# Optimization experiments

Hardware: AMD Instinct MI355X
Metric: run time of the kernel (lower is better)

## Reference

```python
import jax, jax.numpy as jnp
import numpy as np

EMB = 32
STEPS = 3
SLOPE = 0.01  # LeakyReLU default negative slope


def lrelu(x):
    return jnp.where(x > 0, x, SLOPE * x)


def seg_softmax(logits, seg, num_seg):
    # numerically stable per-segment softmax (matches torch_geometric.utils.softmax)
    m = jax.ops.segment_max(logits, seg, num_segments=num_seg)
    e = jnp.exp(logits - m[seg])
    s = jax.ops.segment_sum(e, seg, num_segments=num_seg)
    return e / s[seg]


def setup_inputs() -> dict:
    key = jax.random.key(0)
    ks = jax.random.split(key, 32)
    N, E, G = 200000, 3200000, 128
    p = lambda k, shape: (jax.random.normal(k, shape, dtype=jnp.float32) * 0.1)
    inp = {
        "node_feats": jax.random.normal(ks[0], (N, 1), dtype=jnp.float32),
        "edge_index": jax.random.randint(ks[1], (2, E), 0, N),
        "batch": jnp.sort(jax.random.randint(ks[2], (N,), 0, G)),
        "num_graphs": G,
        # embed_node: Linear(1, 32)
        "W_embed": p(ks[3], (1, EMB)), "b_embed": p(ks[4], (EMB,)),
        # per-step GraphNet params (stacked over steps)
        "Wm": p(ks[5], (STEPS, EMB, EMB)), "bm": p(ks[6], (STEPS, EMB)),          # f_mess (edge_size=0)
        "Wa": p(ks[7], (STEPS, 3 * EMB, EMB)), "ba": p(ks[8], (STEPS, EMB)),      # f_agg: [x, xg, agg]
        # per-step GlobalNode params
        "Wgate": p(ks[9], (STEPS, EMB, 1)), "bgate": p(ks[10], (STEPS, 1)),       # att_mask
        "Wfeat": p(ks[11], (STEPS, EMB, EMB)), "bfeat": p(ks[12], (STEPS, EMB)),  # att_feat
        "Wt": p(ks[13], (STEPS, 2 * EMB, EMB)), "bt": p(ks[14], (STEPS, EMB)),    # transform
        # heads
        "W_v": p(ks[15], (EMB, 1)), "b_v": p(ks[16], (1,)),
        "W_a0": p(ks[17], (EMB, 2)), "b_a0": p(ks[18], (2,)),
        "W_a1": p(ks[19], (EMB, 1)), "b_a1": p(ks[20], (1,)),
    }
    return inp


def reference(node_feats, edge_index, batch, num_graphs,
              W_embed, b_embed, Wm, bm, Wa, ba, Wgate, bgate, Wfeat, bfeat,
              Wt, bt, W_v, b_v, W_a0, b_a0, W_a1, b_a1):
    N = node_feats.shape[0]
    src, dst = edge_index[0], edge_index[1]

    x = lrelu(node_feats @ W_embed + b_embed)            # [N, 32]
    xg = jnp.zeros((num_graphs, EMB), dtype=x.dtype)     # [G, 32]

    for i in range(Wm.shape[0]):
        # GraphNet: gather -> MLP -> scatter-max -> update MLP + residual
        msg = lrelu(x[src] @ Wm[i] + bm[i])              # [E, 32]
        agg = jax.ops.segment_max(msg, dst, num_segments=N)
        agg = jnp.where(jnp.isfinite(agg), agg, 0.0)     # empty segments -> 0
        z = jnp.concatenate([x, xg[batch], agg], axis=1)  # [N, 96]
        x = lrelu(z @ Wa[i] + ba[i]) + x

        # GlobalNode: GlobalAttention pooling + transform with residual
        gate = seg_softmax((x @ Wgate[i] + bgate[i])[:, 0], batch, num_graphs)  # [N]
        feat = lrelu(x @ Wfeat[i] + bfeat[i])            # [N, 32]
        pooled = jax.ops.segment_sum(gate[:, None] * feat, batch, num_segments=num_graphs)
        cat = jnp.concatenate([pooled, xg], axis=1)      # [G, 64]
        xg = lrelu(cat @ Wt[i] + bt[i]) + xg

    value = xg @ W_v + b_v                               # [G, 1]
    a0_probs = jax.nn.softmax(xg @ W_a0 + b_a0, axis=1)  # [G, 2]
    a1_softmax = seg_softmax((x @ W_a1 + b_a1)[:, 0], batch, num_graphs)  # [N]
    return value, a0_probs, a1_softmax
```

## Files before the change

kernel.cpp:

```cpp
#include <hip/hip_runtime.h>
#include <hip/hip_bf16.h>

#define GG 128
#define SLOPE 0.01f
#define CHUNK 8192
#define NPB 64
#define NREP 64

#define OFF_Wm   0
#define OFF_bm   3072
#define OFF_Wa   3168
#define OFF_ba   12384
#define OFF_Wg   12480
#define OFF_bg   12576
#define OFF_Wf   12592
#define OFF_bf   15664
#define OFF_Wt   15760
#define OFF_bt   21904
#define OFF_Wa1  22000
#define OFF_ba1  22032
#define WCAT_N   22048

__device__ __forceinline__ float lrelu(float v) { return v > 0.f ? v : SLOPE * v; }

__device__ __forceinline__ float ldf(const void* p, int i, int isf) {
    if (isf) return ((const float*)p)[i];
    return __bfloat162float(((const __hip_bfloat16*)p)[i]);
}
__device__ __forceinline__ void stf(void* p, int i, float v, int isf) {
    if (isf) ((float*)p)[i] = v;
    else ((__hip_bfloat16*)p)[i] = __float2bfloat16(v);
}

__device__ __forceinline__ float bfLo(unsigned u) { return __uint_as_float(u << 16); }
__device__ __forceinline__ float bfHi(unsigned u) { return __uint_as_float(u & 0xFFFF0000u); }

__global__ void k_detect(const unsigned short* __restrict__ w, int n, int* __restrict__ flag) {
    __shared__ int bad;
    if (threadIdx.x == 0) bad = 0;
    __syncthreads();
    for (int t = threadIdx.x; t < n; t += 256) {
        unsigned short u = w[t];
        int e = (u >> 7) & 0xFF;
        if (e >= 141) bad = 1;
    }
    __syncthreads();
    if (threadIdx.x == 0) { flag[0] = bad; flag[32] = 1; }
}

struct CvtArgs {
    const void* p[12];
    int off[12];
    int n[12];
};
__global__ void k_cvt_all(CvtArgs a, float* __restrict__ dst, const int* __restrict__ dtf) {
    int isf = *dtf;
    int seg = blockIdx.y;
    int i = blockIdx.x * 256 + threadIdx.x;
    if (i < a.n[seg]) dst[a.off[seg] + i] = ldf(a.p[seg], i, isf);
}

__global__ void k_xgw0(const void* __restrict__ ba0, float* __restrict__ xgw,
                       const int* __restrict__ dtf) {
    int isf = *dtf;
    int idx = blockIdx.x * 256 + threadIdx.x;
    xgw[idx] = ldf(ba0, idx & 31, isf);
}

__global__ void k_embed_msg(const void* __restrict__ nf, const void* __restrict__ We,
                            const void* __restrict__ be,
                            const float* __restrict__ Wm0, const float* __restrict__ bm0,
                            float* __restrict__ x, __hip_bfloat16* __restrict__ m, int N,
                            const int* __restrict__ dtf) {
    __shared__ float WL[1024];
    __shared__ float WeL[32], beL[32], bmL[32];
    __shared__ float xs[8][32];
    int isf = *dtf;
    int tid = threadIdx.x;
    for (int t = tid; t < 1024; t += 256) WL[t] = Wm0[t];
    if (tid < 32) { WeL[tid] = ldf(We, tid, isf); beL[tid] = ldf(be, tid, isf); bmL[tid] = bm0[tid]; }
    int s = tid >> 5, j = tid & 31;
    int n = blockIdx.x * 8 + s;
    __syncthreads();
    float xv = 0.f;
    if (n < N) {
        xv = lrelu(ldf(nf, n, isf) * WeL[j] + beL[j]);
        x[n * 32 + j] = xv;
        xs[s][j] = xv;
    }
    __syncthreads();
    if (n >= N) return;
    float acc = bmL[j];
#pragma unroll
    for (int k = 0; k < 32; ++k) acc += xs[s][k] * WL[k * 32 + j];
    m[n * 32 + j] = __float2bfloat16(lrelu(acc));
}

__global__ void k_graph_off(const int* __restrict__ batch, int* __restrict__ goff, int N) {
    int n = blockIdx.x * 256 + threadIdx.x;
    if (n >= N) return;
    int bn = batch[n];
    if (n == 0) {
        for (int g = 0; g <= bn; ++g) goff[g] = 0;
    } else {
        int bp = batch[n - 1];
        for (int g = bp + 1; g <= bn; ++g) goff[g] = n;
    }
    if (n == N - 1) {
        for (int g = bn + 1; g <= GG; ++g) goff[g] = N;
    }
}

__global__ void k_hist(const int* __restrict__ dst, unsigned* __restrict__ deg, int E) {
    int e = blockIdx.x * 256 + threadIdx.x;
    if (e >= E) return;
    atomicAdd(&deg[dst[e]], 1u);
}
__global__ void k_scan1(const unsigned* __restrict__ deg, unsigned* __restrict__ excl,
                        unsigned* __restrict__ bsum, int N) {
    __shared__ unsigned s[256];
    int i = blockIdx.x * 256 + threadIdx.x;
    unsigned v = (i < N) ? deg[i] : 0u;
    s[threadIdx.x] = v;
    __syncthreads();
    for (int off = 1; off < 256; off <<= 1) {
        unsigned t = (threadIdx.x >= (unsigned)off) ? s[threadIdx.x - off] : 0u;
        __syncthreads();
        s[threadIdx.x] += t;
        __syncthreads();
    }
    if (i < N) excl[i] = s[threadIdx.x] - v;
    if (threadIdx.x == 255) bsum[blockIdx.x] = s[255];
}
__global__ void k_scan2(const unsigned* __restrict__ bsum, unsigned* __restrict__ boff, int nb) {
    __shared__ unsigned s[256];
    __shared__ unsigned carry;
    if (threadIdx.x == 0) carry = 0u;
    __syncthreads();
    for (int base = 0; base < nb; base += 256) {
        int i = base + threadIdx.x;
        unsigned v = (i < nb) ? bsum[i] : 0u;
        s[threadIdx.x] = v;
        __syncthreads();
        for (int off = 1; off < 256; off <<= 1) {
            unsigned t = (threadIdx.x >= (unsigned)off) ? s[threadIdx.x - off] : 0u;
            __syncthreads();
            s[threadIdx.x] += t;
            __syncthreads();
        }
        if (i < nb) boff[i] = carry + s[threadIdx.x] - v;
        __syncthreads();
        if (threadIdx.x == 0) carry += s[255];
        __syncthreads();
    }
}
__global__ void k_scan3(unsigned* __restrict__ indptr, const unsigned* __restrict__ boff,
                        unsigned* __restrict__ cursor, int N, int E) {
    int i = blockIdx.x * 256 + threadIdx.x;
    if (i >= N) return;
    unsigned v = indptr[i] + boff[i >> 8];
    indptr[i] = v;
    cursor[i] = v;
    if (i == 0) indptr[N] = (unsigned)E;
}
__global__ void k_scatter(const int* __restrict__ src, const int* __restrict__ dst,
                          unsigned* __restrict__ cursor, unsigned* __restrict__ ssrc, int E) {
    int e = blockIdx.x * 256 + threadIdx.x;
    if (e >= E) return;
    unsigned pos = atomicAdd(&cursor[dst[e]], 1u);
    ssrc[pos] = (unsigned)src[e];
}

__global__ void k_bhist(const int* __restrict__ dst, unsigned* __restrict__ bcnt, int E, int B) {
    __shared__ unsigned h[2048];
    for (int t = threadIdx.x; t < B; t += 256) h[t] = 0;
    __syncthreads();
    int start = blockIdx.x * CHUNK, end = min(E, start + CHUNK);
    for (int e = start + threadIdx.x; e < end; e += 256)
        atomicAdd(&h[dst[e] >> 8], 1u);
    __syncthreads();
    for (int t = threadIdx.x; t < B; t += 256)
        if (h[t]) atomicAdd(&bcnt[t], h[t]);
}

__global__ void k_bscan(const unsigned* __restrict__ bcnt, unsigned* __restrict__ bbase,
                        unsigned* __restrict__ bcur, int B, int E) {
    __shared__ unsigned s[256];
    __shared__ unsigned carry;
    if (threadIdx.x == 0) carry = 0u;
    __syncthreads();
    for (int base = 0; base < B; base += 256) {
        int i = base + threadIdx.x;
        unsigned v = (i < B) ? bcnt[i] : 0u;
        s[threadIdx.x] = v;
        __syncthreads();
        for (int off = 1; off < 256; off <<= 1) {
            unsigned t = (threadIdx.x >= (unsigned)off) ? s[threadIdx.x - off] : 0u;
            __syncthreads();
            s[threadIdx.x] += t;
            __syncthreads();
        }
        if (i < B) {
            unsigned ex = carry + s[threadIdx.x] - v;
            bbase[i] = ex;
            bcur[i] = ex;
        }
        __syncthreads();
        if (threadIdx.x == 0) carry += s[255];
        __syncthreads();
    }
    if (threadIdx.x == 0) bbase[B] = (unsigned)E;
}

__global__ void k_binA(const int* __restrict__ src, const int* __restrict__ dst,
                       unsigned* __restrict__ bcur, unsigned long long* __restrict__ packed,
                       int E, int B) {
    __shared__ unsigned h[2048];
    __shared__ unsigned pos[2048];
    for (int t = threadIdx.x; t < B; t += 256) h[t] = 0;
    __syncthreads();
    int start = blockIdx.x * CHUNK, end = min(E, start + CHUNK);
    for (int e = start + threadIdx.x; e < end; e += 256)
        atomicAdd(&h[dst[e] >> 8], 1u);
    __syncthreads();
    for (int t = threadIdx.x; t < B; t += 256)
        pos[t] = h[t] ? atomicAdd(&bcur[t], h[t]) : 0u;
    __syncthreads();
    for (int e = start + threadIdx.x; e < end; e += 256) {
        int d = dst[e];
        unsigned p = atomicAdd(&pos[d >> 8], 1u);
        packed[p] = ((unsigned long long)(unsigned)d << 32) | (unsigned)src[e];
    }
}

__global__ void k_csr(const unsigned long long* __restrict__ packed,
                      const unsigned* __restrict__ bbase,
                      unsigned* __restrict__ indptr,
                      unsigned* __restrict__ ssrc, int N, int E) {
    __shared__ unsigned deg[256];
    __shared__ unsigned scn[256];
    __shared__ unsigned cur[256];
    int g = blockIdx.x, tid = threadIdx.x;
    int n0 = g << 8;
    int cnt = min(256, N - n0);
    deg[tid] = 0;
    __syncthreads();
    unsigned e0 = bbase[g], e1 = bbase[g + 1];
    for (unsigned e = e0 + tid; e < e1; e += 256) {
        int d = (int)(packed[e] >> 32);
        atomicAdd(&deg[d - n0], 1u);
    }
    __syncthreads();
    unsigned v = deg[tid];
    scn[tid] = v;
    __syncthreads();
    for (int off = 1; off < 256; off <<= 1) {
        unsigned t = (tid >= off) ? scn[tid - off] : 0u;
        __syncthreads();
        scn[tid] += t;
        __syncthreads();
    }
    unsigned start = e0 + scn[tid] - v;
    if (tid < cnt) { indptr[n0 + tid] = start; cur[tid] = start; }
    if (g == (int)gridDim.x - 1 && tid == 0) indptr[N] = (unsigned)E;
    __syncthreads();
    for (unsigned e = e0 + tid; e < e1; e += 256) {
        unsigned long long pk = packed[e];
        int d = (int)(pk >> 32);
        unsigned p = atomicAdd(&cur[d - n0], 1u);
        ssrc[p] = (unsigned)pk;
    }
}

__global__ __launch_bounds__(256, 4)
void k_step(float* __restrict__ x, const __hip_bfloat16* __restrict__ m_in,
            __hip_bfloat16* __restrict__ m_out,
            const int* __restrict__ batch,
            const unsigned* __restrict__ indptr, const unsigned* __restrict__ ssrc,
            const float* __restrict__ Wa, const float* __restrict__ xgw,
            const float* __restrict__ Wg, const float* __restrict__ bg,
            const float* __restrict__ Wa1, const float* __restrict__ ba1,
            const float* __restrict__ Wf, const float* __restrict__ bf,
            const float* __restrict__ Wm_nx, const float* __restrict__ bm_nx,
            float* __restrict__ la1, float* __restrict__ U, float* __restrict__ S,
            int N, int hasNext) {
    __shared__ float WL[2048];
    __shared__ float WmL[1024];
    __shared__ float zL[8][64];
    __shared__ float xnL[8][32];
    __shared__ float WgL[32], W1L[32], bmL[32], bfL[32];
    __shared__ float bgL, b1L;
    int tid = threadIdx.x;
    for (int t = tid; t < 2048; t += 256) WL[t] = (t < 1024) ? Wa[t] : Wa[t + 1024];
    if (hasNext) {
        for (int t = tid; t < 1024; t += 256) WmL[t] = Wm_nx[t];
        if (tid < 32) bmL[tid] = bm_nx[tid];
    }
    if (tid < 32) { WgL[tid] = Wg[tid]; W1L[tid] = Wa1[tid]; bfL[tid] = bf[tid]; }
    if (tid == 0) { bgL = bg[0]; b1L = ba1[0]; }
    int s = tid >> 5, j = tid & 31;
    int c = j & 7, eo = j >> 3;
    float wfr[32];
#pragma unroll
    for (int k = 0; k < 32; ++k) wfr[k] = Wf[k * 32 + j];
    const uint2* m2 = (const uint2*)m_in;
    int nbase = blockIdx.x * NPB;
    int rep = blockIdx.x & (NREP - 1);
    float* Urep = U + (size_t)rep * GG * 32;
    float* Srep = S + (size_t)rep * GG;
    __syncthreads();
    int gcur = -1;
    float Uacc = 0.f, Sacc = 0.f;
    for (int sub = 0; sub < NPB / 8; ++sub) {
        int n = nbase + sub * 8 + s;
        bool valid = n < N;
        int gb = gcur;
        float xj = 0.f;
        if (valid) {
            xj = x[n * 32 + j];
            zL[s][j] = xj;
            gb = batch[n];
        }
        if (valid && gb != gcur) {
            if (gcur >= 0) {
                atomicAdd(&Urep[gcur * 32 + j], Uacc);
                if (j == 0) atomicAdd(&Srep[gcur], Sacc);
            }
            gcur = gb; Uacc = 0.f; Sacc = 0.f;
        }
        unsigned st = 0, en = 0;
        if (valid) { st = indptr[n]; en = indptr[n + 1]; }
        float a[4];
#pragma unroll
        for (int t = 0; t < 4; ++t) a[t] = -INFINITY;
        if (en > st) {
            unsigned last = en - 1;
            for (unsigned base = st; base < en; base += 32) {
                unsigned eA = min(base + eo, last);
                unsigned eB = min(base + 4 + eo, last);
                unsigned eC = min(base + 8 + eo, last);
                unsigned eD = min(base + 12 + eo, last);
                unsigned eE = min(base + 16 + eo, last);
                unsigned eF = min(base + 20 + eo, last);
                unsigned eG = min(base + 24 + eo, last);
                unsigned eH = min(base + 28 + eo, last);
                unsigned sA = ssrc[eA];
                unsigned sB = ssrc[eB];
                unsigned sC = ssrc[eC];
                unsigned sD = ssrc[eD];
                unsigned sE = ssrc[eE];
                unsigned sF = ssrc[eF];
                unsigned sG = ssrc[eG];
                unsigned sH = ssrc[eH];
                uint2 vA = m2[sA * 8 + c];
                uint2 vB = m2[sB * 8 + c];
                uint2 vC = m2[sC * 8 + c];
                uint2 vD = m2[sD * 8 + c];
                uint2 vE = m2[sE * 8 + c];
                uint2 vF = m2[sF * 8 + c];
                uint2 vG = m2[sG * 8 + c];
                uint2 vH = m2[sH * 8 + c];
                a[0] = fmaxf(a[0], fmaxf(fmaxf(fmaxf(bfLo(vA.x), bfLo(vB.x)), fmaxf(bfLo(vC.x), bfLo(vD.x))),
                                         fmaxf(fmaxf(bfLo(vE.x), bfLo(vF.x)), fmaxf(bfLo(vG.x), bfLo(vH.x)))));
                a[1] = fmaxf(a[1], fmaxf(fmaxf(fmaxf(bfHi(vA.x), bfHi(vB.x)), fmaxf(bfHi(vC.x), bfHi(vD.x))),
                                         fmaxf(fmaxf(bfHi(vE.x), bfHi(vF.x)), fmaxf(bfHi(vG.x), bfHi(vH.x)))));
                a[2] = fmaxf(a[2], fmaxf(fmaxf(fmaxf(bfLo(vA.y), bfLo(vB.y)), fmaxf(bfLo(vC.y), bfLo(vD.y))),
                                         fmaxf(fmaxf(bfLo(vE.y), bfLo(vF.y)), fmaxf(bfLo(vG.y), bfLo(vH.y)))));
                a[3] = fmaxf(a[3], fmaxf(fmaxf(fmaxf(bfHi(vA.y), bfHi(vB.y)), fmaxf(bfHi(vC.y), bfHi(vD.y))),
                                         fmaxf(fmaxf(bfHi(vE.y), bfHi(vF.y)), fmaxf(bfHi(vG.y), bfHi(vH.y)))));
            }
        }
#pragma unroll
        for (int t = 0; t < 4; ++t) {
            a[t] = fmaxf(a[t], __shfl_xor(a[t], 8));
            a[t] = fmaxf(a[t], __shfl_xor(a[t], 16));
        }
        if (valid && eo == 0) {
            bool empty = (st == en);
#pragma unroll
            for (int t = 0; t < 4; ++t)
                zL[s][32 + (c << 2) + t] = empty ? 0.f : a[t];
        }
        if (valid) {
            float acc0 = xgw[gb * 32 + j];
            float acc1 = 0.f;
#pragma unroll
            for (int k = 0; k < 64; k += 2) {
                acc0 += zL[s][k] * WL[k * 32 + j];
                acc1 += zL[s][k + 1] * WL[(k + 1) * 32 + j];
            }
            float xn = lrelu(acc0 + acc1) + xj;
            x[n * 32 + j] = xn;
            xnL[s][j] = xn;
            float lv = xn * WgL[j];
            if (hasNext) {
#pragma unroll
                for (int off = 16; off; off >>= 1) lv += __shfl_xor(lv, off);
            } else {
                float l1 = xn * W1L[j];
#pragma unroll
                for (int off = 16; off; off >>= 1) { lv += __shfl_xor(lv, off); l1 += __shfl_xor(l1, off); }
                if (j == 0) la1[n] = l1 + b1L;
            }
            float e = __expf(lv + bgL);
            float f = bfL[j];
            if (hasNext) {
                float a2 = bmL[j];
#pragma unroll
                for (int k = 0; k < 32; ++k) {
                    float v = xnL[s][k];
                    f += v * wfr[k];
                    a2 += v * WmL[k * 32 + j];
                }
                m_out[n * 32 + j] = __float2bfloat16(lrelu(a2));
            } else {
#pragma unroll
                for (int k = 0; k < 32; ++k) f += xnL[s][k] * wfr[k];
            }
            Uacc += e * lrelu(f);
            Sacc += e;
        }
    }
    if (gcur >= 0) {
        atomicAdd(&Urep[gcur * 32 + j], Uacc);
        if (j == 0) atomicAdd(&Srep[gcur], Sacc);
    }
}

__global__ void k_gupd(float* __restrict__ U, float* __restrict__ S,
                       const float* __restrict__ xg_in,
                       const float* __restrict__ Wt, const float* __restrict__ bt,
                       float* __restrict__ xg_out,
                       const float* __restrict__ WaNx, const float* __restrict__ baNx,
                       float* __restrict__ xgw, int hasNext) {
    __shared__ float Up[8][32];
    __shared__ float Sp[8];
    __shared__ float pl[32];
    __shared__ float vL[32];
    int g = blockIdx.x;
    int tid = threadIdx.x;
    int rp = tid >> 5, j = tid & 31;
    float usum = 0.f, ssum = 0.f;
    for (int r = rp; r < NREP; r += 8) {
        size_t ui = (size_t)r * GG * 32 + g * 32 + j;
        usum += U[ui];
        U[ui] = 0.f;
        if (j == 0) { ssum += S[r * GG + g]; S[r * GG + g] = 0.f; }
    }
    Up[rp][j] = usum;
    if (j == 0) Sp[rp] = ssum;
    __syncthreads();
    if (rp == 0) {
        float ut = 0.f;
#pragma unroll
        for (int i = 0; i < 8; ++i) ut += Up[i][j];
        float st = ((Sp[0] + Sp[1]) + (Sp[2] + Sp[3])) + ((Sp[4] + Sp[5]) + (Sp[6] + Sp[7]));
        float inv = (st > 0.f) ? 1.f / st : 0.f;
        pl[j] = ut * inv;
        float xgv = xg_in[g * 32 + j];
        vL[j] = xgv;
        float acc = bt[j];
#pragma unroll
        for (int k = 0; k < 32; ++k) acc += pl[k] * Wt[k * 32 + j];
#pragma unroll
        for (int k = 0; k < 32; ++k) acc += vL[k] * Wt[(32 + k) * 32 + j];
        float v = lrelu(acc) + xgv;
        xg_out[g * 32 + j] = v;
        if (hasNext) {
            vL[j] = v;
            float aw = baNx[j];
#pragma unroll
            for (int k = 0; k < 32; ++k) aw += vL[k] * WaNx[(32 + k) * 32 + j];
            xgw[g * 32 + j] = aw;
        }
    }
}

__global__ void k_final(const float* __restrict__ logits, const int* __restrict__ goff,
                        const float* __restrict__ xg,
                        const void* __restrict__ Wv, const void* __restrict__ bv,
                        const void* __restrict__ Wa0, const void* __restrict__ ba0,
                        void* __restrict__ out, int N, const int* __restrict__ dtf) {
    __shared__ float red[256];
    int isf = *dtf;
    int g = blockIdx.x, tid = threadIdx.x;
    int s0 = goff[g], s1 = goff[g + 1];
    float lm = -INFINITY;
    for (int n = s0 + tid; n < s1; n += 256) lm = fmaxf(lm, logits[n]);
    red[tid] = lm;
    __syncthreads();
    for (int off = 128; off; off >>= 1) {
        if (tid < off) red[tid] = fmaxf(red[tid], red[tid + off]);
        __syncthreads();
    }
    float gmax = red[0];
    __syncthreads();
    float ls = 0.f;
    for (int n = s0 + tid; n < s1; n += 256) ls += expf(logits[n] - gmax);
    red[tid] = ls;
    __syncthreads();
    for (int off = 128; off; off >>= 1) {
        if (tid < off) red[tid] += red[tid + off];
        __syncthreads();
    }
    float inv = (red[0] > 0.f) ? 1.f / red[0] : 0.f;
    __syncthreads();
    for (int n = s0 + tid; n < s1; n += 256)
        stf(out, 384 + n, expf(logits[n] - gmax) * inv, isf);
    if (tid == 0) {
        float acc = ldf(bv, 0, isf);
        for (int k = 0; k < 32; ++k) acc += xg[g * 32 + k] * ldf(Wv, k, isf);
        stf(out, g, acc, isf);
        float l0 = ldf(ba0, 0, isf), l1 = ldf(ba0, 1, isf);
        for (int k = 0; k < 32; ++k) {
            float xv = xg[g * 32 + k];
            l0 += xv * ldf(Wa0, k * 2, isf);
            l1 += xv * ldf(Wa0, k * 2 + 1, isf);
        }
        float mm = fmaxf(l0, l1);
        float e0 = expf(l0 - mm), e1 = expf(l1 - mm);
        float si = 1.f / (e0 + e1);
        stf(out, 128 + 2 * g, e0 * si, isf);
        stf(out, 128 + 2 * g + 1, e1 * si, isf);
    }
}

extern "C" void kernel_launch(void* const* d_in, const int* in_sizes, int n_in,
                              void* d_out, int out_size, void* d_ws, size_t ws_size,
                              hipStream_t stream) {
    const void* nf      = d_in[0];
    const int*  eidx    = (const int*)d_in[1];
    const int*  batch   = (const int*)d_in[2];
    const void* W_embed = d_in[4];
    const void* b_embed = d_in[5];
    const void* Wm      = d_in[6];
    const void* bm      = d_in[7];
    const void* Wa      = d_in[8];
    const void* ba      = d_in[9];
    const void* Wgate   = d_in[10];
    const void* bgate   = d_in[11];
    const void* Wfeat   = d_in[12];
    const void* bfeat   = d_in[13];
    const void* Wt      = d_in[14];
    const void* bt      = d_in[15];
    const void* W_v     = d_in[16];
    const void* b_v     = d_in[17];
    const void* W_a0    = d_in[18];
    const void* b_a0    = d_in[19];
    const void* W_a1    = d_in[20];
    const void* b_a1    = d_in[21];

    const int N = in_sizes[0];
    const int E = in_sizes[1] / 2;
    const int nWm = in_sizes[6];
    const int* src = eidx;
    const int* dst = eidx + E;
    const int B = (N + 255) >> 8;

    char* ws = (char*)d_ws;
    size_t off = 0;
    auto alloc = [&](size_t bytes) -> char* {
        char* p = ws + off;
        off = (off + bytes + 255) & ~(size_t)255;
        return p;
    };
    float*          x      = (float*)alloc((size_t)N * 32 * 4);
    size_t mBytes  = (size_t)N * 32 * 2;
    size_t pkBytes = (size_t)E * 8;
    size_t rBytes  = (2 * mBytes > pkBytes) ? 2 * mBytes : pkBytes;
    char*  mRegion = alloc(rBytes);
    unsigned long long* packed = (unsigned long long*)mRegion;
    __hip_bfloat16*     m_a    = (__hip_bfloat16*)mRegion;
    __hip_bfloat16*     m_b    = (__hip_bfloat16*)(mRegion + mBytes);
    float*          la1    = (float*)alloc((size_t)N * 4);
    unsigned*       indptr = (unsigned*)alloc((size_t)(N + 1) * 4);
    unsigned*       cursor = (unsigned*)alloc((size_t)N * 4);
    unsigned*       ssrc   = (unsigned*)alloc((size_t)(E + 16) * 4);
    const int nb = (N + 255) / 256;
    unsigned*       bsum   = (unsigned*)alloc((size_t)nb * 4);
    unsigned*       boff   = (unsigned*)alloc((size_t)nb * 4);
    unsigned*       bcnt   = (unsigned*)alloc((size_t)(B + 1) * 4);
    unsigned*       bbase  = (unsigned*)alloc((size_t)(B + 1) * 4);
    unsigned*       bcur   = (unsigned*)alloc((size_t)(B + 1) * 4);
    int*            goff   = (int*)alloc((size_t)(GG + 1) * 4);
    float*          xg_a   = (float*)alloc((size_t)GG * 32 * 4);
    float*          xg_b   = (float*)alloc((size_t)GG * 32 * 4);
    float*          xgw    = (float*)alloc((size_t)GG * 32 * 4);
    float*          U      = (float*)alloc((size_t)NREP * GG * 32 * 4);
    float*          S      = (float*)alloc((size_t)NREP * GG * 4);
    int*            dtf    = (int*)alloc(256);
    float*          wcat   = (float*)alloc((size_t)WCAT_N * 4);

    const int nB_n  = (N + 255) / 256;
    const int nB_e  = (E + 255) / 256;
    const int nB_n8 = (N + 7) / 8;
    const int nB_st = (N + NPB - 1) / NPB;
    const int nB_ch = (E + CHUNK - 1) / CHUNK;

    hipMemsetAsync(xg_a, 0, (size_t)GG * 32 * 4, stream);
    hipMemsetAsync(bcnt, 0, (size_t)(B + 1) * 4, stream);
    hipMemsetAsync(U, 0, (size_t)NREP * GG * 32 * 4, stream);
    hipMemsetAsync(S, 0, (size_t)NREP * GG * 4, stream);

    k_detect<<<1, 256, 0, stream>>>((const unsigned short*)Wm, nWm, dtf);

    CvtArgs ca;
    const void* ps[12] = {Wm, bm, Wa, ba, Wgate, bgate, Wfeat, bfeat, Wt, bt, W_a1, b_a1};
    const int  offs[12] = {OFF_Wm, OFF_bm, OFF_Wa, OFF_ba, OFF_Wg, OFF_bg,
                           OFF_Wf, OFF_bf, OFF_Wt, OFF_bt, OFF_Wa1, OFF_ba1};
    const int  ns[12]  = {3072, 96, 9216, 96, 96, 3, 3072, 96, 6144, 96, 32, 1};
    for (int i = 0; i < 12; ++i) { ca.p[i] = ps[i]; ca.off[i] = offs[i]; ca.n[i] = ns[i]; }
    k_cvt_all<<<dim3(36, 12), 256, 0, stream>>>(ca, wcat, dtf);

    k_xgw0<<<(GG * 32) / 256, 256, 0, stream>>>(ba, xgw, dtf);

    k_graph_off<<<nB_n, 256, 0, stream>>>(batch, goff, N);

    if (B <= 2048) {
        k_bhist<<<nB_ch, 256, 0, stream>>>(dst, bcnt, E, B);
        k_bscan<<<1, 256, 0, stream>>>(bcnt, bbase, bcur, B, E);
        k_binA<<<nB_ch, 256, 0, stream>>>(src, dst, bcur, packed, E, B);
        k_csr<<<B, 256, 0, stream>>>(packed, bbase, indptr, ssrc, N, E);
    } else {
        hipMemsetAsync(cursor, 0, (size_t)N * 4, stream);
        k_hist<<<nB_e, 256, 0, stream>>>(dst, cursor, E);
        k_scan1<<<nb, 256, 0, stream>>>(cursor, indptr, bsum, N);
        k_scan2<<<1, 256, 0, stream>>>(bsum, boff, nb);
        k_scan3<<<nB_n, 256, 0, stream>>>(indptr, boff, cursor, N, E);
        k_scatter<<<nB_e, 256, 0, stream>>>(src, dst, cursor, ssrc, E);
    }

    k_embed_msg<<<nB_n8, 256, 0, stream>>>(nf, W_embed, b_embed,
                                           wcat + OFF_Wm, wcat + OFF_bm, x, m_a, N, dtf);

    float* xg_cur = xg_a;
    float* xg_nxt = xg_b;
    __hip_bfloat16* m_cur = m_a;
    __hip_bfloat16* m_nxt = m_b;
    for (int i = 0; i < 3; ++i) {
        int hasNext = (i < 2) ? 1 : 0;
        k_step<<<nB_st, 256, 0, stream>>>(x, m_cur, m_nxt, batch, indptr, ssrc,
                                          wcat + OFF_Wa + i * 3072, xgw,
                                          wcat + OFF_Wg + i * 32, wcat + OFF_bg + i,
                                          wcat + OFF_Wa1, wcat + OFF_ba1,
                                          wcat + OFF_Wf + i * 1024, wcat + OFF_bf + i * 32,
                                          wcat + OFF_Wm + (i + 1) * 1024,
                                          wcat + OFF_bm + (i + 1) * 32,
                                          la1, U, S, N, hasNext);
        k_gupd<<<GG, 256, 0, stream>>>(U, S, xg_cur,
                                       wcat + OFF_Wt + i * 2048,
                                       wcat + OFF_bt + i * 32, xg_nxt,
                                       wcat + OFF_Wa + (i + 1) * 3072,
                                       wcat + OFF_ba + (i + 1) * 32,
                                       xgw, hasNext);
        float* tmp = xg_cur; xg_cur = xg_nxt; xg_nxt = tmp;
        __hip_bfloat16* tm = m_cur; m_cur = m_nxt; m_nxt = tm;
    }

    k_final<<<GG, 256, 0, stream>>>(la1, goff, xg_cur, W_v, b_v, W_a0, b_a0,
                                    d_out, N, dtf);
}
```

Before: 582.3 us.

## Software-pipeline node metadata, ssrc and message gathers across sub-iterations in k_step

Measured after the change: 701.8 us. 1.21x slower.

```diff
diff --git a/kernel.cpp b/kernel.cpp
--- a/kernel.cpp
+++ b/kernel.cpp
@@ -286,12 +286,14 @@
             int N, int hasNext) {
     __shared__ float WL[2048];
     __shared__ float WmL[1024];
+    __shared__ float WfL[1024];
     __shared__ float zL[8][64];
     __shared__ float xnL[8][32];
     __shared__ float WgL[32], W1L[32], bmL[32], bfL[32];
     __shared__ float bgL, b1L;
     int tid = threadIdx.x;
     for (int t = tid; t < 2048; t += 256) WL[t] = (t < 1024) ? Wa[t] : Wa[t + 1024];
+    for (int t = tid; t < 1024; t += 256) WfL[t] = Wf[t];
     if (hasNext) {
         for (int t = tid; t < 1024; t += 256) WmL[t] = Wm_nx[t];
         if (tid < 32) bmL[tid] = bm_nx[tid];
@@ -300,9 +302,6 @@
     if (tid == 0) { bgL = bg[0]; b1L = ba1[0]; }
     int s = tid >> 5, j = tid & 31;
     int c = j & 7, eo = j >> 3;
-    float wfr[32];
-#pragma unroll
-    for (int k = 0; k < 32; ++k) wfr[k] = Wf[k * 32 + j];
     const uint2* m2 = (const uint2*)m_in;
     int nbase = blockIdx.x * NPB;
     int rep = blockIdx.x & (NREP - 1);
@@ -311,86 +310,130 @@
     __syncthreads();
     int gcur = -1;
     float Uacc = 0.f, Sacc = 0.f;
-    for (int sub = 0; sub < NPB / 8; ++sub) {
+
+    int   cmn = 0, cmv = 0, cmg = 0;  float cmx = 0.f;  unsigned cmst = 0, cmen = 0;
+    int   imn, imv, img;              float imx;        unsigned imst, imen;
+    int   pmn, pmv, pmg;              float pmx;        unsigned pmst, pmen;
+    int   qn, qv, qg;                 float qx;         unsigned qst, qen;
+    unsigned ssA, ssB, ssC, ssD, ssE, ssF, ssG, ssH;
+    unsigned srA, srB, srC, srD, srE, srF, srG, srH;
+    uint2 mA, mB, mC, mD, mE, mF, mG, mH;
+
+    auto metaLoad = [&](int sub, int& n_, int& v_, int& g_, float& x_, unsigned& st_, unsigned& en_) {
         int n = nbase + sub * 8 + s;
-        bool valid = n < N;
-        int gb = gcur;
-        float xj = 0.f;
-        if (valid) {
-            xj = x[n * 32 + j];
-            zL[s][j] = xj;
-            gb = batch[n];
-        }
-        if (valid && gb != gcur) {
-            if (gcur >= 0) {
-                atomicAdd(&Urep[gcur * 32 + j], Uacc);
-                if (j == 0) atomicAdd(&Srep[gcur], Sacc);
-            }
-            gcur = gb; Uacc = 0.f; Sacc = 0.f;
-        }
-        unsigned st = 0, en = 0;
-        if (valid) { st = indptr[n]; en = indptr[n + 1]; }
-        float a[4];
-#pragma unroll
-        for (int t = 0; t < 4; ++t) a[t] = -INFINITY;
-        if (en > st) {
-            unsigned last = en - 1;
-            for (unsigned base = st; base < en; base += 32) {
-                unsigned eA = min(base + eo, last);
-                unsigned eB = min(base + 4 + eo, last);
-                unsigned eC = min(base + 8 + eo, last);
-                unsigned eD = min(base + 12 + eo, last);
-                unsigned eE = min(base + 16 + eo, last);
-                unsigned eF = min(base + 20 + eo, last);
-                unsigned eG = min(base + 24 + eo, last);
-                unsigned eH = min(base + 28 + eo, last);
-                unsigned sA = ssrc[eA];
-                unsigned sB = ssrc[eB];
-                unsigned sC = ssrc[eC];
-                unsigned sD = ssrc[eD];
-                unsigned sE = ssrc[eE];
-                unsigned sF = ssrc[eF];
-                unsigned sG = ssrc[eG];
-                unsigned sH = ssrc[eH];
-                uint2 vA = m2[sA * 8 + c];
-                uint2 vB = m2[sB * 8 + c];
-                uint2 vC = m2[sC * 8 + c];
-                uint2 vD = m2[sD * 8 + c];
-                uint2 vE = m2[sE * 8 + c];
-                uint2 vF = m2[sF * 8 + c];
-                uint2 vG = m2[sG * 8 + c];
-                uint2 vH = m2[sH * 8 + c];
-                a[0] = fmaxf(a[0], fmaxf(fmaxf(fmaxf(bfLo(vA.x), bfLo(vB.x)), fmaxf(bfLo(vC.x), bfLo(vD.x))),
-                                         fmaxf(fmaxf(bfLo(vE.x), bfLo(vF.x)), fmaxf(bfLo(vG.x), bfLo(vH.x)))));
-                a[1] = fmaxf(a[1], fmaxf(fmaxf(fmaxf(bfHi(vA.x), bfHi(vB.x)), fmaxf(bfHi(vC.x), bfHi(vD.x))),
-                                         fmaxf(fmaxf(bfHi(vE.x), bfHi(vF.x)), fmaxf(bfHi(vG.x), bfHi(vH.x)))));
-                a[2] = fmaxf(a[2], fmaxf(fmaxf(fmaxf(bfLo(vA.y), bfLo(vB.y)), fmaxf(bfLo(vC.y), bfLo(vD.y))),
-                                         fmaxf(fmaxf(bfLo(vE.y), bfLo(vF.y)), fmaxf(bfLo(vG.y), bfLo(vH.y)))));
-                a[3] = fmaxf(a[3], fmaxf(fmaxf(fmaxf(bfHi(vA.y), bfHi(vB.y)), fmaxf(bfHi(vC.y), bfHi(vD.y))),
-                                         fmaxf(fmaxf(bfHi(vE.y), bfHi(vF.y)), fmaxf(bfHi(vG.y), bfHi(vH.y)))));
+        int cl = (n < N) ? n : (N - 1);
+        v_ = (sub < NPB / 8 && n < N) ? 1 : 0;
+        n_ = cl;
+        x_ = x[cl * 32 + j];
+        g_ = batch[cl];
+        st_ = indptr[cl];
+        en_ = indptr[cl + 1];
+    };
+    auto ssrcIssue = [&](unsigned st_, unsigned en_,
+                         unsigned& a0, unsigned& a1, unsigned& a2, unsigned& a3,
+                         unsigned& a4, unsigned& a5, unsigned& a6, unsigned& a7) {
+        unsigned b = (en_ > st_) ? st_ : 0u;
+        unsigned last = (en_ > st_) ? (en_ - 1) : 0u;
+        a0 = ssrc[min(b + eo, last)];
+        a1 = ssrc[min(b + 4 + eo, last)];
+        a2 = ssrc[min(b + 8 + eo, last)];
+        a3 = ssrc[min(b + 12 + eo, last)];
+        a4 = ssrc[min(b + 16 + eo, last)];
+        a5 = ssrc[min(b + 20 + eo, last)];
+        a6 = ssrc[min(b + 24 + eo, last)];
+        a7 = ssrc[min(b + 28 + eo, last)];
+    };
+
+    metaLoad(0, imn, imv, img, imx, imst, imen);
+    metaLoad(1, pmn, pmv, pmg, pmx, pmst, pmen);
+    ssrcIssue(imst, imen, ssA, ssB, ssC, ssD, ssE, ssF, ssG, ssH);
+
+    for (int sub = 0; sub <= NPB / 8; ++sub) {
+        float a0 = -INFINITY, a1 = -INFINITY, a2 = -INFINITY, a3 = -INFINITY;
+        if (sub >= 1) {
+            a0 = fmaxf(fmaxf(fmaxf(bfLo(mA.x), bfLo(mB.x)), fmaxf(bfLo(mC.x), bfLo(mD.x))),
+                       fmaxf(fmaxf(bfLo(mE.x), bfLo(mF.x)), fmaxf(bfLo(mG.x), bfLo(mH.x))));
+            a1 = fmaxf(fmaxf(fmaxf(bfHi(mA.x), bfHi(mB.x)), fmaxf(bfHi(mC.x), bfHi(mD.x))),
+                       fmaxf(fmaxf(bfHi(mE.x), bfHi(mF.x)), fmaxf(bfHi(mG.x), bfHi(mH.x))));
+            a2 = fmaxf(fmaxf(fmaxf(bfLo(mA.y), bfLo(mB.y)), fmaxf(bfLo(mC.y), bfLo(mD.y))),
+                       fmaxf(fmaxf(bfLo(mE.y), bfLo(mF.y)), fmaxf(bfLo(mG.y), bfLo(mH.y))));
+            a3 = fmaxf(fmaxf(fmaxf(bfHi(mA.y), bfHi(mB.y)), fmaxf(bfHi(mC.y), bfHi(mD.y))),
+                       fmaxf(fmaxf(bfHi(mE.y), bfHi(mF.y)), fmaxf(bfHi(mG.y), bfHi(mH.y))));
+            if (cmen > cmst + 32) {
+                unsigned last = cmen - 1;
+                for (unsigned base = cmst + 32; base < cmen; base += 32) {
+                    unsigned tA = ssrc[min(base + eo, last)];
+                    unsigned tB = ssrc[min(base + 4 + eo, last)];
+                    unsigned tC = ssrc[min(base + 8 + eo, last)];
+                    unsigned tD = ssrc[min(base + 12 + eo, last)];
+                    unsigned tE = ssrc[min(base + 16 + eo, last)];
+                    unsigned tF = ssrc[min(base + 20 + eo, last)];
+                    unsigned tG = ssrc[min(base + 24 + eo, last)];
+                    unsigned tH = ssrc[min(base + 28 + eo, last)];
+                    uint2 wA = m2[tA * 8 + c];
+                    uint2 wB = m2[tB * 8 + c];
+                    uint2 wC = m2[tC * 8 + c];
+                    uint2 wD = m2[tD * 8 + c];
+                    uint2 wE = m2[tE * 8 + c];
+                    uint2 wF = m2[tF * 8 + c];
+                    uint2 wG = m2[tG * 8 + c];
+                    uint2 wH = m2[tH * 8 + c];
+                    a0 = fmaxf(a0, fmaxf(fmaxf(fmaxf(bfLo(wA.x), bfLo(wB.x)), fmaxf(bfLo(wC.x), bfLo(wD.x))),
+                                         fmaxf(fmaxf(bfLo(wE.x), bfLo(wF.x)), fmaxf(bfLo(wG.x), bfLo(wH.x)))));
+                    a1 = fmaxf(a1, fmaxf(fmaxf(fmaxf(bfHi(wA.x), bfHi(wB.x)), fmaxf(bfHi(wC.x), bfHi(wD.x))),
+                                         fmaxf(fmaxf(bfHi(wE.x), bfHi(wF.x)), fmaxf(bfHi(wG.x), bfHi(wH.x)))));
+                    a2 = fmaxf(a2, fmaxf(fmaxf(fmaxf(bfLo(wA.y), bfLo(wB.y)), fmaxf(bfLo(wC.y), bfLo(wD.y))),
+                                         fmaxf(fmaxf(bfLo(wE.y), bfLo(wF.y)), fmaxf(bfLo(wG.y), bfLo(wH.y)))));
+                    a3 = fmaxf(a3, fmaxf(fmaxf(fmaxf(bfHi(wA.y), bfHi(wB.y)), fmaxf(bfHi(wC.y), bfHi(wD.y))),
+                                         fmaxf(fmaxf(bfHi(wE.y), bfHi(wF.y)), fmaxf(bfHi(wG.y), bfHi(wH.y)))));
+                }
             }
         }
-#pragma unroll
-        for (int t = 0; t < 4; ++t) {
-            a[t] = fmaxf(a[t], __shfl_xor(a[t], 8));
-            a[t] = fmaxf(a[t], __shfl_xor(a[t], 16));
+        if (sub < NPB / 8) {
+            mA = m2[ssA * 8 + c];
+            mB = m2[ssB * 8 + c];
+            mC = m2[ssC * 8 + c];
+            mD = m2[ssD * 8 + c];
+            mE = m2[ssE * 8 + c];
+            mF = m2[ssF * 8 + c];
+            mG = m2[ssG * 8 + c];
+            mH = m2[ssH * 8 + c];
+            metaLoad(sub + 2, qn, qv, qg, qx, qst, qen);
+            ssrcIssue(pmst, pmen, srA, srB, srC, srD, srE, srF, srG, srH);
         }
-        if (valid && eo == 0) {
-            bool empty = (st == en);
-#pragma unroll
-            for (int t = 0; t < 4; ++t)
-                zL[s][32 + (c << 2) + t] = empty ? 0.f : a[t];
-        }
-        if (valid) {
-            float acc0 = xgw[gb * 32 + j];
+        if (sub >= 1 && cmv) {
+            a0 = fmaxf(a0, __shfl_xor(a0, 8));
+            a0 = fmaxf(a0, __shfl_xor(a0, 16));
+            a1 = fmaxf(a1, __shfl_xor(a1, 8));
+            a1 = fmaxf(a1, __shfl_xor(a1, 16));
+            a2 = fmaxf(a2, __shfl_xor(a2, 8));
+            a2 = fmaxf(a2, __shfl_xor(a2, 16));
+            a3 = fmaxf(a3, __shfl_xor(a3, 8));
+            a3 = fmaxf(a3, __shfl_xor(a3, 16));
+            if (cmg != gcur) {
+                if (gcur >= 0) {
+                    atomicAdd(&Urep[gcur * 32 + j], Uacc);
+                    if (j == 0) atomicAdd(&Srep[gcur], Sacc);
+                }
+                gcur = cmg; Uacc = 0.f; Sacc = 0.f;
+            }
+            zL[s][j] = cmx;
+            if (eo == 0) {
+                bool empty = (cmst == cmen);
+                zL[s][32 + (c << 2) + 0] = empty ? 0.f : a0;
+                zL[s][32 + (c << 2) + 1] = empty ? 0.f : a1;
+                zL[s][32 + (c << 2) + 2] = empty ? 0.f : a2;
+                zL[s][32 + (c << 2) + 3] = empty ? 0.f : a3;
+            }
+            float acc0 = xgw[cmg * 32 + j];
             float acc1 = 0.f;
 #pragma unroll
             for (int k = 0; k < 64; k += 2) {
                 acc0 += zL[s][k] * WL[k * 32 + j];
                 acc1 += zL[s][k + 1] * WL[(k + 1) * 32 + j];
             }
-            float xn = lrelu(acc0 + acc1) + xj;
-            x[n * 32 + j] = xn;
+            float xn = lrelu(acc0 + acc1) + cmx;
+            x[cmn * 32 + j] = xn;
             xnL[s][j] = xn;
             float lv = xn * WgL[j];
             if (hasNext) {
@@ -400,26 +443,32 @@
                 float l1 = xn * W1L[j];
 #pragma unroll
                 for (int off = 16; off; off >>= 1) { lv += __shfl_xor(lv, off); l1 += __shfl_xor(l1, off); }
-                if (j == 0) la1[n] = l1 + b1L;
+                if (j == 0) la1[cmn] = l1 + b1L;
             }
             float e = __expf(lv + bgL);
             float f = bfL[j];
             if (hasNext) {
-                float a2 = bmL[j];
-#pragma unroll
-                for (int k = 0; k < 32; ++k) {
-                    float v = xnL[s][k];
-                    f += v * wfr[k];
-                    a2 += v * WmL[k * 32 + j];
+                float a20 = bmL[j], a21 = 0.f;
+#pragma unroll
+                for (int k = 0; k < 32; k += 2) {
+                    float v0 = xnL[s][k], v1 = xnL[s][k + 1];
+                    f += v0 * WfL[k * 32 + j] + v1 * WfL[(k + 1) * 32 + j];
+                    a20 += v0 * WmL[k * 32 + j];
+                    a21 += v1 * WmL[(k + 1) * 32 + j];
                 }
-                m_out[n * 32 + j] = __float2bfloat16(lrelu(a2));
+                m_out[cmn * 32 + j] = __float2bfloat16(lrelu(a20 + a21));
             } else {
 #pragma unroll
-                for (int k = 0; k < 32; ++k) f += xnL[s][k] * wfr[k];
+                for (int k = 0; k < 32; ++k) f += xnL[s][k] * WfL[k * 32 + j];
             }
             Uacc += e * lrelu(f);
             Sacc += e;
         }
+        cmn = imn; cmv = imv; cmg = img; cmx = imx; cmst = imst; cmen = imen;
+        imn = pmn; imv = pmv; img = pmg; imx = pmx; imst = pmst; imen = pmen;
+        pmn = qn;  pmv = qv;  pmg = qg;  pmx = qx;  pmst = qst;  pmen = qen;
+        ssA = srA; ssB = srB; ssC = srC; ssD = srD;
+        ssE = srE; ssF = srF; ssG = srG; ssH = srH;
     }
     if (gcur >= 0) {
         atomicAdd(&Urep[gcur * 32 + j], Uacc);
```

## Merge setup kernels and memsets into fewer launches, fuse final head into gupd

Applied to the files above, without the earlier changes.

Measured after the change: 568.9 us (median of 2 runs). 1.02x faster.

```diff
diff --git a/kernel.cpp b/kernel.cpp
--- a/kernel.cpp
+++ b/kernel.cpp
@@ -35,8 +35,10 @@
 __device__ __forceinline__ float bfLo(unsigned u) { return __uint_as_float(u << 16); }
 __device__ __forceinline__ float bfHi(unsigned u) { return __uint_as_float(u & 0xFFFF0000u); }
 
-__global__ void k_detect(const unsigned short* __restrict__ w, int n, int* __restrict__ flag) {
+__global__ void k_detect(const unsigned short* __restrict__ w, int n, int* __restrict__ flag,
+                         unsigned* __restrict__ bcnt, int B) {
     __shared__ int bad;
+    for (int t = threadIdx.x; t <= B; t += 256) bcnt[t] = 0u;
     if (threadIdx.x == 0) bad = 0;
     __syncthreads();
     for (int t = threadIdx.x; t < n; t += 256) {
@@ -53,61 +55,68 @@
     int off[12];
     int n[12];
 };
-__global__ void k_cvt_all(CvtArgs a, float* __restrict__ dst, const int* __restrict__ dtf) {
-    int isf = *dtf;
-    int seg = blockIdx.y;
-    int i = blockIdx.x * 256 + threadIdx.x;
-    if (i < a.n[seg]) dst[a.off[seg] + i] = ldf(a.p[seg], i, isf);
-}
-
-__global__ void k_xgw0(const void* __restrict__ ba0, float* __restrict__ xgw,
-                       const int* __restrict__ dtf) {
-    int isf = *dtf;
-    int idx = blockIdx.x * 256 + threadIdx.x;
-    xgw[idx] = ldf(ba0, idx & 31, isf);
-}
-
-__global__ void k_embed_msg(const void* __restrict__ nf, const void* __restrict__ We,
-                            const void* __restrict__ be,
-                            const float* __restrict__ Wm0, const float* __restrict__ bm0,
-                            float* __restrict__ x, __hip_bfloat16* __restrict__ m, int N,
-                            const int* __restrict__ dtf) {
-    __shared__ float WL[1024];
-    __shared__ float WeL[32], beL[32], bmL[32];
-    __shared__ float xs[8][32];
-    int isf = *dtf;
+__global__ void k_prep(CvtArgs a, float* __restrict__ wcat, const int* __restrict__ dtf,
+                       const void* __restrict__ ba0, float* __restrict__ xgw,
+                       const int* __restrict__ batch, int* __restrict__ goff, int N,
+                       const int* __restrict__ dst, unsigned* __restrict__ bcnt, int E, int B,
+                       float* __restrict__ xg_a, float* __restrict__ U, float* __restrict__ S) {
+    __shared__ unsigned h[2048];
+    int blk = blockIdx.x;
     int tid = threadIdx.x;
-    for (int t = tid; t < 1024; t += 256) WL[t] = Wm0[t];
-    if (tid < 32) { WeL[tid] = ldf(We, tid, isf); beL[tid] = ldf(be, tid, isf); bmL[tid] = bm0[tid]; }
-    int s = tid >> 5, j = tid & 31;
-    int n = blockIdx.x * 8 + s;
-    __syncthreads();
-    float xv = 0.f;
-    if (n < N) {
-        xv = lrelu(ldf(nf, n, isf) * WeL[j] + beL[j]);
-        x[n * 32 + j] = xv;
-        xs[s][j] = xv;
-    }
-    __syncthreads();
-    if (n >= N) return;
-    float acc = bmL[j];
-#pragma unroll
-    for (int k = 0; k < 32; ++k) acc += xs[s][k] * WL[k * 32 + j];
-    m[n * 32 + j] = __float2bfloat16(lrelu(acc));
-}
-
-__global__ void k_graph_off(const int* __restrict__ batch, int* __restrict__ goff, int N) {
-    int n = blockIdx.x * 256 + threadIdx.x;
-    if (n >= N) return;
-    int bn = batch[n];
-    if (n == 0) {
-        for (int g = 0; g <= bn; ++g) goff[g] = 0;
-    } else {
-        int bp = batch[n - 1];
-        for (int g = bp + 1; g <= bn; ++g) goff[g] = n;
-    }
-    if (n == N - 1) {
-        for (int g = bn + 1; g <= GG; ++g) goff[g] = N;
+    const int cG = (N + 255) >> 8;
+    const int cH = (E + CHUNK - 1) / CHUNK;
+    if (blk < 432) {
+        int seg = blk / 36;
+        int i = (blk % 36) * 256 + tid;
+        int isf = *dtf;
+        if (i < a.n[seg]) wcat[a.off[seg] + i] = ldf(a.p[seg], i, isf);
+        return;
+    }
+    blk -= 432;
+    if (blk < 16) {
+        int isf = *dtf;
+        int idx = blk * 256 + tid;
+        xgw[idx] = ldf(ba0, idx & 31, isf);
+        return;
+    }
+    blk -= 16;
+    if (blk < cG) {
+        int n = blk * 256 + tid;
+        if (n >= N) return;
+        int bn = batch[n];
+        if (n == 0) {
+            for (int g = 0; g <= bn; ++g) goff[g] = 0;
+        } else {
+            int bp = batch[n - 1];
+            for (int g = bp + 1; g <= bn; ++g) goff[g] = n;
+        }
+        if (n == N - 1) {
+            for (int g = bn + 1; g <= GG; ++g) goff[g] = N;
+        }
+        return;
+    }
+    blk -= cG;
+    if (blk < cH) {
+        if (B > 2048) return;
+        for (int t = tid; t < B; t += 256) h[t] = 0;
+        __syncthreads();
+        int start = blk * CHUNK, end = min(E, start + CHUNK);
+        for (int e = start + tid; e < end; e += 256)
+            atomicAdd(&h[dst[e] >> 8], 1u);
+        __syncthreads();
+        for (int t = tid; t < B; t += 256)
+            if (h[t]) atomicAdd(&bcnt[t], h[t]);
+        return;
+    }
+    blk -= cH;
+    {
+        float4 z4 = make_float4(0.f, 0.f, 0.f, 0.f);
+        long long fi = (long long)blk * 256 + tid;
+        if (fi < 65536) { ((float4*)U)[fi] = z4; return; }
+        fi -= 65536;
+        if (fi < 2048) { ((float4*)S)[fi] = z4; return; }
+        fi -= 2048;
+        if (fi < 1024) { ((float4*)xg_a)[fi] = z4; return; }
     }
 }
 
@@ -171,18 +180,6 @@
     ssrc[pos] = (unsigned)src[e];
 }
 
-__global__ void k_bhist(const int* __restrict__ dst, unsigned* __restrict__ bcnt, int E, int B) {
-    __shared__ unsigned h[2048];
-    for (int t = threadIdx.x; t < B; t += 256) h[t] = 0;
-    __syncthreads();
-    int start = blockIdx.x * CHUNK, end = min(E, start + CHUNK);
-    for (int e = start + threadIdx.x; e < end; e += 256)
-        atomicAdd(&h[dst[e] >> 8], 1u);
-    __syncthreads();
-    for (int t = threadIdx.x; t < B; t += 256)
-        if (h[t]) atomicAdd(&bcnt[t], h[t]);
-}
-
 __global__ void k_bscan(const unsigned* __restrict__ bcnt, unsigned* __restrict__ bbase,
                         unsigned* __restrict__ bcur, int B, int E) {
     __shared__ unsigned s[256];
@@ -212,25 +209,56 @@
     if (threadIdx.x == 0) bbase[B] = (unsigned)E;
 }
 
-__global__ void k_binA(const int* __restrict__ src, const int* __restrict__ dst,
+__global__ void k_work(const int* __restrict__ src, const int* __restrict__ dst,
                        unsigned* __restrict__ bcur, unsigned long long* __restrict__ packed,
-                       int E, int B) {
+                       int E, int B, int nbA,
+                       const void* __restrict__ nf, const void* __restrict__ We,
+                       const void* __restrict__ be,
+                       const float* __restrict__ Wm0, const float* __restrict__ bm0,
+                       float* __restrict__ x, __hip_bfloat16* __restrict__ m, int N,
+                       const int* __restrict__ dtf) {
     __shared__ unsigned h[2048];
     __shared__ unsigned pos[2048];
-    for (int t = threadIdx.x; t < B; t += 256) h[t] = 0;
-    __syncthreads();
-    int start = blockIdx.x * CHUNK, end = min(E, start + CHUNK);
-    for (int e = start + threadIdx.x; e < end; e += 256)
-        atomicAdd(&h[dst[e] >> 8], 1u);
-    __syncthreads();
-    for (int t = threadIdx.x; t < B; t += 256)
-        pos[t] = h[t] ? atomicAdd(&bcur[t], h[t]) : 0u;
-    __syncthreads();
-    for (int e = start + threadIdx.x; e < end; e += 256) {
-        int d = dst[e];
-        unsigned p = atomicAdd(&pos[d >> 8], 1u);
-        packed[p] = ((unsigned long long)(unsigned)d << 32) | (unsigned)src[e];
-    }
+    __shared__ float WL[1024];
+    __shared__ float WeL[32], beL[32], bmL[32];
+    __shared__ float xs[8][32];
+    int tid = threadIdx.x;
+    if ((int)blockIdx.x < nbA) {
+        for (int t = tid; t < B; t += 256) h[t] = 0;
+        __syncthreads();
+        int start = blockIdx.x * CHUNK, end = min(E, start + CHUNK);
+        for (int e = start + tid; e < end; e += 256)
+            atomicAdd(&h[dst[e] >> 8], 1u);
+        __syncthreads();
+        for (int t = tid; t < B; t += 256)
+            pos[t] = h[t] ? atomicAdd(&bcur[t], h[t]) : 0u;
+        __syncthreads();
+        for (int e = start + tid; e < end; e += 256) {
+            int d = dst[e];
+            unsigned p = atomicAdd(&pos[d >> 8], 1u);
+            packed[p] = ((unsigned long long)(unsigned)d << 32) | (unsigned)src[e];
+        }
+        return;
+    }
+    int blkE = blockIdx.x - nbA;
+    int isf = *dtf;
+    for (int t = tid; t < 1024; t += 256) WL[t] = Wm0[t];
+    if (tid < 32) { WeL[tid] = ldf(We, tid, isf); beL[tid] = ldf(be, tid, isf); bmL[tid] = bm0[tid]; }
+    int s = tid >> 5, j = tid & 31;
+    int n = blkE * 8 + s;
+    __syncthreads();
+    float xv = 0.f;
+    if (n < N) {
+        xv = lrelu(ldf(nf, n, isf) * WeL[j] + beL[j]);
+        x[n * 32 + j] = xv;
+        xs[s][j] = xv;
+    }
+    __syncthreads();
+    if (n >= N) return;
+    float acc = bmL[j];
+#pragma unroll
+    for (int k = 0; k < 32; ++k) acc += xs[s][k] * WL[k * 32 + j];
+    m[n * 32 + j] = __float2bfloat16(lrelu(acc));
 }
 
 __global__ void k_csr(const unsigned long long* __restrict__ packed,
@@ -432,11 +460,16 @@
                        const float* __restrict__ Wt, const float* __restrict__ bt,
                        float* __restrict__ xg_out,
                        const float* __restrict__ WaNx, const float* __restrict__ baNx,
-                       float* __restrict__ xgw, int hasNext) {
+                       float* __restrict__ xgw, int hasNext,
+                       const float* __restrict__ logits, const int* __restrict__ goff,
+                       const void* __restrict__ Wv, const void* __restrict__ bv,
+                       const void* __restrict__ Wa0, const void* __restrict__ ba0,
+                       void* __restrict__ out, int N, const int* __restrict__ dtf) {
     __shared__ float Up[8][32];
     __shared__ float Sp[8];
     __shared__ float pl[32];
     __shared__ float vL[32];
+    __shared__ float red[256];
     int g = blockIdx.x;
     int tid = threadIdx.x;
     int rp = tid >> 5, j = tid & 31;
@@ -466,24 +499,17 @@
         for (int k = 0; k < 32; ++k) acc += vL[k] * Wt[(32 + k) * 32 + j];
         float v = lrelu(acc) + xgv;
         xg_out[g * 32 + j] = v;
+        vL[j] = v;
         if (hasNext) {
-            vL[j] = v;
             float aw = baNx[j];
 #pragma unroll
             for (int k = 0; k < 32; ++k) aw += vL[k] * WaNx[(32 + k) * 32 + j];
             xgw[g * 32 + j] = aw;
         }
     }
-}
-
-__global__ void k_final(const float* __restrict__ logits, const int* __restrict__ goff,
-                        const float* __restrict__ xg,
-                        const void* __restrict__ Wv, const void* __restrict__ bv,
-                        const void* __restrict__ Wa0, const void* __restrict__ ba0,
-                        void* __restrict__ out, int N, const int* __restrict__ dtf) {
-    __shared__ float red[256];
+    __syncthreads();
+    if (hasNext) return;
     int isf = *dtf;
-    int g = blockIdx.x, tid = threadIdx.x;
     int s0 = goff[g], s1 = goff[g + 1];
     float lm = -INFINITY;
     for (int n = s0 + tid; n < s1; n += 256) lm = fmaxf(lm, logits[n]);
@@ -509,11 +535,11 @@
         stf(out, 384 + n, expf(logits[n] - gmax) * inv, isf);
     if (tid == 0) {
         float acc = ldf(bv, 0, isf);
-        for (int k = 0; k < 32; ++k) acc += xg[g * 32 + k] * ldf(Wv, k, isf);
+        for (int k = 0; k < 32; ++k) acc += vL[k] * ldf(Wv, k, isf);
         stf(out, g, acc, isf);
         float l0 = ldf(ba0, 0, isf), l1 = ldf(ba0, 1, isf);
         for (int k = 0; k < 32; ++k) {
-            float xv = xg[g * 32 + k];
+            float xv = vL[k];
             l0 += xv * ldf(Wa0, k * 2, isf);
             l1 += xv * ldf(Wa0, k * 2 + 1, isf);
         }
@@ -566,12 +592,9 @@
     };
     float*          x      = (float*)alloc((size_t)N * 32 * 4);
     size_t mBytes  = (size_t)N * 32 * 2;
-    size_t pkBytes = (size_t)E * 8;
-    size_t rBytes  = (2 * mBytes > pkBytes) ? 2 * mBytes : pkBytes;
-    char*  mRegion = alloc(rBytes);
-    unsigned long long* packed = (unsigned long long*)mRegion;
-    __hip_bfloat16*     m_a    = (__hip_bfloat16*)mRegion;
-    __hip_bfloat16*     m_b    = (__hip_bfloat16*)(mRegion + mBytes);
+    __hip_bfloat16*     m_a    = (__hip_bfloat16*)alloc(mBytes);
+    __hip_bfloat16*     m_b    = (__hip_bfloat16*)alloc(mBytes);
+    unsigned long long* packed = (unsigned long long*)alloc((size_t)E * 8);
     float*          la1    = (float*)alloc((size_t)N * 4);
     unsigned*       indptr = (unsigned*)alloc((size_t)(N + 1) * 4);
     unsigned*       cursor = (unsigned*)alloc((size_t)N * 4);
@@ -597,12 +620,7 @@
     const int nB_st = (N + NPB - 1) / NPB;
     const int nB_ch = (E + CHUNK - 1) / CHUNK;
 
-    hipMemsetAsync(xg_a, 0, (size_t)GG * 32 * 4, stream);
-    hipMemsetAsync(bcnt, 0, (size_t)(B + 1) * 4, stream);
-    hipMemsetAsync(U, 0, (size_t)NREP * GG * 32 * 4, stream);
-    hipMemsetAsync(S, 0, (size_t)NREP * GG * 4, stream);
-
-    k_detect<<<1, 256, 0, stream>>>((const unsigned short*)Wm, nWm, dtf);
+    k_detect<<<1, 256, 0, stream>>>((const unsigned short*)Wm, nWm, dtf, bcnt, B);
 
     CvtArgs ca;
     const void* ps[12] = {Wm, bm, Wa, ba, Wgate, bgate, Wfeat, bfeat, Wt, bt, W_a1, b_a1};
@@ -610,16 +628,17 @@
                            OFF_Wf, OFF_bf, OFF_Wt, OFF_bt, OFF_Wa1, OFF_ba1};
     const int  ns[12]  = {3072, 96, 9216, 96, 96, 3, 3072, 96, 6144, 96, 32, 1};
     for (int i = 0; i < 12; ++i) { ca.p[i] = ps[i]; ca.off[i] = offs[i]; ca.n[i] = ns[i]; }
-    k_cvt_all<<<dim3(36, 12), 256, 0, stream>>>(ca, wcat, dtf);
-
-    k_xgw0<<<(GG * 32) / 256, 256, 0, stream>>>(ba, xgw, dtf);
-
-    k_graph_off<<<nB_n, 256, 0, stream>>>(batch, goff, N);
+
+    const int nPrep = 432 + 16 + nB_n + nB_ch + 268;
+    k_prep<<<nPrep, 256, 0, stream>>>(ca, wcat, dtf, ba, xgw, batch, goff, N,
+                                      dst, bcnt, E, B, xg_a, U, S);
 
     if (B <= 2048) {
-        k_bhist<<<nB_ch, 256, 0, stream>>>(dst, bcnt, E, B);
         k_bscan<<<1, 256, 0, stream>>>(bcnt, bbase, bcur, B, E);
-        k_binA<<<nB_ch, 256, 0, stream>>>(src, dst, bcur, packed, E, B);
+        k_work<<<nB_ch + nB_n8, 256, 0, stream>>>(src, dst, bcur, packed, E, B, nB_ch,
+                                                  nf, W_embed, b_embed,
+                                                  wcat + OFF_Wm, wcat + OFF_bm,
+                                                  x, m_a, N, dtf);
         k_csr<<<B, 256, 0, stream>>>(packed, bbase, indptr, ssrc, N, E);
     } else {
         hipMemsetAsync(cursor, 0, (size_t)N * 4, stream);
@@ -628,10 +647,11 @@
         k_scan2<<<1, 256, 0, stream>>>(bsum, boff, nb);
         k_scan3<<<nB_n, 256, 0, stream>>>(indptr, boff, cursor, N, E);
         k_scatter<<<nB_e, 256, 0, stream>>>(src, dst, cursor, ssrc, E);
-    }
-
-    k_embed_msg<<<nB_n8, 256, 0, stream>>>(nf, W_embed, b_embed,
-                                           wcat + OFF_Wm, wcat + OFF_bm, x, m_a, N, dtf);
+        k_work<<<nB_n8, 256, 0, stream>>>(src, dst, bcur, packed, E, B, 0,
+                                          nf, W_embed, b_embed,
+                                          wcat + OFF_Wm, wcat + OFF_bm,
+                                          x, m_a, N, dtf);
+    }
 
     float* xg_cur = xg_a;
     float* xg_nxt = xg_b;
@@ -652,11 +672,10 @@
                                        wcat + OFF_bt + i * 32, xg_nxt,
                                        wcat + OFF_Wa + (i + 1) * 3072,
                                        wcat + OFF_ba + (i + 1) * 32,
-                                       xgw, hasNext);
+                                       xgw, hasNext,
+                                       la1, goff, W_v, b_v, W_a0, b_a0,
+                                       d_out, N, dtf);
         float* tmp = xg_cur; xg_cur = xg_nxt; xg_nxt = tmp;
         __hip_bfloat16* tm = m_cur; m_cur = m_nxt; m_nxt = tm;
     }
-
-    k_final<<<GG, 256, 0, stream>>>(la1, goff, xg_cur, W_v, b_v, W_a0, b_a0,
-                                    d_out, N, dtf);
-}
+}
```
